# Performance work log

Hardware: AMD Instinct MI355X
Metric: run time of the kernel (lower is better)

## Reference

```python
import jax, jax.numpy as jnp
import numpy as np

HEAD_SIZE = 64
N_EMBD = 128
B, T = 16, 2048


def setup_inputs() -> dict:
    key = jax.random.key(0)
    ks = jax.random.split(key, 7)
    s = 1.0 / np.sqrt(N_EMBD)
    return {
        "x": jax.random.normal(ks[0], (B, T, N_EMBD), dtype=jnp.float32),
        "Wk": jax.random.normal(ks[1], (N_EMBD, HEAD_SIZE), dtype=jnp.float32) * s,
        "bk": jax.random.normal(ks[2], (HEAD_SIZE,), dtype=jnp.float32) * s,
        "Wq": jax.random.normal(ks[3], (N_EMBD, HEAD_SIZE), dtype=jnp.float32) * s,
        "bq": jax.random.normal(ks[4], (HEAD_SIZE,), dtype=jnp.float32) * s,
        "Wv": jax.random.normal(ks[5], (N_EMBD, HEAD_SIZE), dtype=jnp.float32) * s,
        "bv": jax.random.normal(ks[6], (HEAD_SIZE,), dtype=jnp.float32) * s,
    }


def reference(x, Wk, bk, Wq, bq, Wv, bv):
    # x: [B, T, C]; single-head causal attention (dropout in eval mode = identity)
    Tdim = x.shape[1]
    k = x @ Wk + bk  # [B, T, H]
    q = x @ Wq + bq  # [B, T, H]
    v = x @ Wv + bv  # [B, T, H]
    scale = jnp.asarray(k.shape[-1], x.dtype) ** -0.5
    wei = jnp.einsum("bth,bsh->bts", q, k) * scale  # [B, T, T]
    causal = jnp.tril(jnp.ones((Tdim, Tdim), dtype=bool))
    wei = jnp.where(causal, wei, -jnp.inf)
    wei = jax.nn.softmax(wei, axis=-1)
    out = jnp.einsum("bts,bsh->bth", wei, v)  # [B, T, H]
    return out
```

## Files before the change

kernel.cpp:

```cpp
#include <hip/hip_runtime.h>
#include <hip/hip_bf16.h>
#include <math.h>

#define HS 64
#define NE 128
#define TSEQ 2048

typedef short s8v __attribute__((ext_vector_type(8)));
typedef float f4v __attribute__((ext_vector_type(4)));

__device__ __forceinline__ unsigned short f2bf(float f) {
    unsigned int u = __float_as_uint(f);
    u += 0x7FFFu + ((u >> 16) & 1u);
    return (unsigned short)(u >> 16);
}

__device__ __forceinline__ unsigned int pkbf(float a, float b) {
    union { __hip_bfloat162 h; unsigned int u; } cv;
    cv.h = __float22bfloat162_rn(make_float2(a, b));
    return cv.u;
}

__device__ __forceinline__ s8v mk_s8v(unsigned int a, unsigned int b,
                                      unsigned int c, unsigned int d) {
    union { unsigned int u[4]; s8v v; } cv;
    cv.u[0] = a; cv.u[1] = b; cv.u[2] = c; cv.u[3] = d;
    return cv.v;
}

__device__ __forceinline__ float fexp2(float x) {
    float r;
    asm("v_exp_f32 %0, %1" : "=v"(r) : "v"(x));
    return r;
}

__device__ __forceinline__ void glds16(const unsigned short* g, unsigned short* l) {
    __builtin_amdgcn_global_load_lds(
        (const __attribute__((address_space(1))) unsigned int*)g,
        (__attribute__((address_space(3))) unsigned int*)l,
        16, 0, 0);
}

__global__ __launch_bounds__(256) void wconv(
    const float* __restrict__ Wq, const float* __restrict__ Wk,
    const float* __restrict__ Wv, unsigned short* __restrict__ wt)
{
    const int g = blockIdx.x * 256 + threadIdx.x;
    const int lane = g & 63;
    const int mtks = g >> 6;
    const int mt = mtks >> 2;
    const int ks = mtks & 3;
    const int li = lane & 15;
    const int quad = lane >> 4;
    const int m = mt * 16 + li;
    const int mat = m >> 6;
    const int n = m & 63;
    const int k0 = ks * 32 + quad * 8;
    const float* W = (mat == 0) ? Wq : (mat == 1) ? Wk : Wv;
    const float s = (mat == 0) ? 0.18033688f : 1.0f;

    unsigned int u[4];
#pragma unroll
    for (int h = 0; h < 4; ++h)
        u[h] = pkbf(W[(k0 + 2 * h) * HS + n] * s, W[(k0 + 2 * h + 1) * HS + n] * s);
    *(s8v*)(wt + (size_t)g * 8) = mk_s8v(u[0], u[1], u[2], u[3]);
}

__global__ __launch_bounds__(64) void qkv(
    const float* __restrict__ x, const unsigned short* __restrict__ wt,
    const float* __restrict__ bq, const float* __restrict__ bk,
    const float* __restrict__ bv,
    unsigned short* __restrict__ qo, unsigned short* __restrict__ ko,
    unsigned short* __restrict__ vt)
{
    const int tid = threadIdx.x;
    const int quad = tid >> 4;
    const int li = tid & 15;
    const size_t t0 = (size_t)blockIdx.x * 16;
    const size_t t = t0 + li;

    s8v xb[4];
    const float* xr = x + t * NE + quad * 8;
#pragma unroll
    for (int ks = 0; ks < 4; ++ks) {
        float4 f0 = *(const float4*)(xr + ks * 32);
        float4 f1 = *(const float4*)(xr + ks * 32 + 4);
        xb[ks] = mk_s8v(pkbf(f0.x, f0.y), pkbf(f0.z, f0.w),
                        pkbf(f1.x, f1.y), pkbf(f1.z, f1.w));
    }

    f4v acc[12];
#pragma unroll
    for (int mt = 0; mt < 12; ++mt) acc[mt] = (f4v){0.f, 0.f, 0.f, 0.f};

#pragma unroll
    for (int mt = 0; mt < 12; ++mt) {
#pragma unroll
        for (int ks = 0; ks < 4; ++ks) {
            s8v af = *(const s8v*)(wt + ((mt * 4 + ks) << 9) + tid * 8);
            acc[mt] = __builtin_amdgcn_mfma_f32_16x16x32_bf16(af, xb[ks], acc[mt], 0, 0, 0);
        }
    }

    const int d0 = quad * 4;
    const float sq = 0.18033688f;

#pragma unroll
    for (int mt = 0; mt < 4; ++mt) {
        float4 bb = *(const float4*)(bq + mt * 16 + d0);
        *(ushort4*)(qo + t * HS + mt * 16 + d0) = (ushort4){
            f2bf(acc[mt][0] + bb.x * sq), f2bf(acc[mt][1] + bb.y * sq),
            f2bf(acc[mt][2] + bb.z * sq), f2bf(acc[mt][3] + bb.w * sq)};
    }
#pragma unroll
    for (int mt = 0; mt < 4; ++mt) {
        float4 bb = *(const float4*)(bk + mt * 16 + d0);
        *(ushort4*)(ko + t * HS + mt * 16 + d0) = (ushort4){
            f2bf(acc[mt + 4][0] + bb.x), f2bf(acc[mt + 4][1] + bb.y),
            f2bf(acc[mt + 4][2] + bb.z), f2bf(acc[mt + 4][3] + bb.w)};
    }
    const size_t bidx = t0 >> 11;
    const size_t trow = t & 2047;
#pragma unroll
    for (int mt = 0; mt < 4; ++mt) {
        float4 bb = *(const float4*)(bv + mt * 16 + d0);
#pragma unroll
        for (int r = 0; r < 4; ++r) {
            vt[(bidx * HS + mt * 16 + d0 + r) * TSEQ + trow] =
                f2bf(acc[mt + 8][r] + (&bb.x)[r]);
        }
    }
}

__global__ __launch_bounds__(256) void attn_main(
    const unsigned short* __restrict__ qb,
    const unsigned short* __restrict__ kb,
    const unsigned short* __restrict__ vtb,
    float* __restrict__ out, float* __restrict__ pbuf, float* __restrict__ lsbuf)
{
    __shared__ unsigned short Ks[2][64 * 64];
    __shared__ unsigned short Vs[2][64 * 64];
    __shared__ __align__(16) unsigned short Ps[4][1024];

    const int tid = threadIdx.x;
    const int w = tid >> 6;
    const int lane = tid & 63;
    const int quad = lane >> 4;
    const int li = lane & 15;

    const int id = blockIdx.x;
    const int b = id / 80;
    const int u = 79 - (id - b * 80);
    int qt, c, nc;
    if (u < 8)       { qt = u;                 c = 0;            nc = 1; }
    else if (u < 24) { qt = 8 + ((u - 8) >> 1);  c = (u - 8) & 1;  nc = 2; }
    else if (u < 48) { qt = 16 + (u - 24) / 3;   c = (u - 24) % 3; nc = 3; }
    else             { qt = 24 + ((u - 48) >> 2); c = (u - 48) & 3; nc = 4; }
    const int tb = c * 8;
    const int te_ = tb + 8;
    const int te = (te_ < qt + 1) ? te_ : (qt + 1);

    const size_t base = (size_t)b * TSEQ;
    const int t0 = qt << 6;
    const int qrow = t0 + w * 16 + li;

    const unsigned short* qrp = qb + (base + qrow) * HS + quad * 8;
    s8v qf0 = *(const s8v*)qrp;
    s8v qf1 = *(const s8v*)(qrp + 32);

    const int rA = w * 8 + (lane >> 3);
    const int csw = (lane & 7) ^ (rA & 7);
    const unsigned short* kgA = kb + (base + rA) * HS + csw * 8;
    const unsigned short* kgB = kgA + 32 * HS;
    const unsigned short* vgA = vtb + ((size_t)b * HS + rA) * TSEQ + csw * 8;
    const unsigned short* vgB = vgA + 32 * TSEQ;
    const int ldsA = w * 512 + lane * 8;
    const int ldsB = 2048 + w * 512 + lane * 8;

    glds16(kgA + (size_t)tb * 4096, &Ks[0][ldsA]);
    glds16(kgB + (size_t)tb * 4096, &Ks[0][ldsB]);
    glds16(vgA + (size_t)tb * 64,   &Vs[0][ldsA]);
    glds16(vgB + (size_t)tb * 64,   &Vs[0][ldsB]);

    f4v c_o[4];
#pragma unroll
    for (int f = 0; f < 4; ++f) c_o[f] = (f4v){0.f, 0.f, 0.f, 0.f};
    float lsum = 0.f;

    char* pbse = (char*)&Ps[w][0];
    const int swz0 = (quad ^ (li & 7)) * 8;
    const int swz1 = ((4 + quad) ^ (li & 7)) * 8;

    __syncthreads();

    for (int tl = tb; tl < te; ++tl) {
        const int bi = (tl - tb) & 1;
        if (tl + 1 < te) {
            const int nb = bi ^ 1;
            glds16(kgA + (size_t)(tl + 1) * 4096, &Ks[nb][ldsA]);
            glds16(kgB + (size_t)(tl + 1) * 4096, &Ks[nb][ldsB]);
            glds16(vgA + (size_t)(tl + 1) * 64,   &Vs[nb][ldsA]);
            glds16(vgB + (size_t)(tl + 1) * 64,   &Vs[nb][ldsB]);
        }
        const unsigned short* Kc = &Ks[bi][0];
        const unsigned short* Vc = &Vs[bi][0];
        const bool diag = (tl == qt);

        float pr[4][4];
        float rs = 0.f;
#pragma unroll
        for (int kt = 0; kt < 4; ++kt) {
            const unsigned short* krow = Kc + (kt * 16 + li) * 64;
            s8v k0 = *(const s8v*)(krow + swz0);
            s8v k1 = *(const s8v*)(krow + swz1);
            f4v cst = (f4v){0.f, 0.f, 0.f, 0.f};
            cst = __builtin_amdgcn_mfma_f32_16x16x32_bf16(k0, qf0, cst, 0, 0, 0);
            cst = __builtin_amdgcn_mfma_f32_16x16x32_bf16(k1, qf1, cst, 0, 0, 0);
            if (diag) {
                const int key0 = (tl << 6) + kt * 16 + quad * 4;
#pragma unroll
                for (int rr = 0; rr < 4; ++rr)
                    if (key0 + rr > qrow) cst[rr] = -INFINITY;
            }
#pragma unroll
            for (int rr = 0; rr < 4; ++rr) {
                pr[kt][rr] = fexp2(cst[rr]);
                rs += pr[kt][rr];
            }
        }
        lsum += rs;

#pragma unroll
        for (int kt = 0; kt < 4; ++kt) {
            *(uint2*)(pbse + (kt * 2 + (quad >> 1)) * 256 + li * 16 + (quad & 1) * 8) =
                make_uint2(pkbf(pr[kt][0], pr[kt][1]), pkbf(pr[kt][2], pr[kt][3]));
        }
        s8v pf0 = *(const s8v*)(pbse + lane * 16);
        s8v pf1 = *(const s8v*)(pbse + 1024 + lane * 16);

#pragma unroll
        for (int f = 0; f < 4; ++f) {
            const unsigned short* vrow = Vc + (f * 16 + li) * 64;
            s8v v0 = *(const s8v*)(vrow + swz0);
            s8v v1 = *(const s8v*)(vrow + swz1);
            c_o[f] = __builtin_amdgcn_mfma_f32_16x16x32_bf16(v0, pf0, c_o[f], 0, 0, 0);
            c_o[f] = __builtin_amdgcn_mfma_f32_16x16x32_bf16(v1, pf1, c_o[f], 0, 0, 0);
        }

        __syncthreads();
    }

    lsum += __shfl_xor(lsum, 16);
    lsum += __shfl_xor(lsum, 32);

    if (nc == 1) {
        const float inv = 1.0f / lsum;
        float* orow = out + (base + qrow) * HS + quad * 4;
#pragma unroll
        for (int f = 0; f < 4; ++f) {
            f4v res = c_o[f];
            res[0] *= inv; res[1] *= inv; res[2] *= inv; res[3] *= inv;
            *(f4v*)(orow + f * 16) = res;
        }
    } else {
        const int local = (qt < 16) ? (qt - 8) * 2 + c
                        : (qt < 24) ? 16 + (qt - 16) * 3 + c
                                    : 40 + (qt - 24) * 4 + c;
        const int pidx = b * 72 + local;
        float* pc = pbuf + (size_t)pidx * 4096 + (w * 16 + li) * 64;
#pragma unroll
        for (int f = 0; f < 4; ++f)
            *(f4v*)(pc + f * 16 + quad * 4) = c_o[f];
        if (quad == 0)
            lsbuf[(size_t)pidx * 64 + w * 16 + li] = lsum;
    }
}

__global__ __launch_bounds__(256) void attn_reduce(
    const float* __restrict__ pbuf, const float* __restrict__ lsbuf,
    float* __restrict__ out)
{
    const int g = blockIdx.x;
    const int b = g / 24;
    const int r = g - b * 24;
    int qt, lbase, nc;
    if (r < 8)       { qt = 8 + r;        lbase = 2 * r;            nc = 2; }
    else if (r < 16) { qt = 16 + (r - 8); lbase = 16 + 3 * (r - 8); nc = 3; }
    else             { qt = 24 + (r - 16); lbase = 40 + 4 * (r - 16); nc = 4; }
    const int pidx0 = b * 72 + lbase;

    const int tid = threadIdx.x;
    const int row = tid >> 2;
    const int seg = tid & 3;

    float4 acc[4];
#pragma unroll
    for (int j = 0; j < 4; ++j) acc[j] = make_float4(0.f, 0.f, 0.f, 0.f);
    float ls = 0.f;

    for (int cc = 0; cc < nc; ++cc) {
        const float* pc = pbuf + (size_t)(pidx0 + cc) * 4096 + row * 64 + seg * 16;
#pragma unroll
        for (int j = 0; j < 4; ++j) {
            float4 v = *(const float4*)(pc + j * 4);
            acc[j].x += v.x; acc[j].y += v.y; acc[j].z += v.z; acc[j].w += v.w;
        }
        ls += lsbuf[(size_t)(pidx0 + cc) * 64 + row];
    }
    const float inv = 1.0f / ls;
    float* orow = out + ((size_t)b * TSEQ + (qt << 6) + row) * HS + seg * 16;
#pragma unroll
    for (int j = 0; j < 4; ++j) {
        *(float4*)(orow + j * 4) = make_float4(acc[j].x * inv, acc[j].y * inv,
                                               acc[j].z * inv, acc[j].w * inv);
    }
}

extern "C" void kernel_launch(void* const* d_in, const int* in_sizes, int n_in,
                              void* d_out, int out_size, void* d_ws, size_t ws_size,
                              hipStream_t stream) {
    const float* x  = (const float*)d_in[0];
    const float* Wk = (const float*)d_in[1];
    const float* bk = (const float*)d_in[2];
    const float* Wq = (const float*)d_in[3];
    const float* bq = (const float*)d_in[4];
    const float* Wv = (const float*)d_in[5];
    const float* bv = (const float*)d_in[6];
    float* outp = (float*)d_out;

    const size_t elems = (size_t)16 * TSEQ * HS;
    unsigned short* qbuf = (unsigned short*)d_ws;
    unsigned short* kbuf = qbuf + elems;
    unsigned short* vbuf = kbuf + elems;
    unsigned short* wtb  = vbuf + elems;
    float* pbuf  = (float*)(wtb + 32768);
    float* lsbuf = pbuf + (size_t)1152 * 4096;

    wconv<<<12, 256, 0, stream>>>(Wq, Wk, Wv, wtb);
    qkv<<<2048, 64, 0, stream>>>(x, wtb, bq, bk, bv, qbuf, kbuf, vbuf);
    attn_main<<<1280, 256, 0, stream>>>(qbuf, kbuf, vbuf, outp, pbuf, lsbuf);
    attn_reduce<<<384, 256, 0, stream>>>(pbuf, lsbuf, outp);
}
```

Measured before the change: 117.3 us.

## Fuse split-KV reduction into attention kernel via last-block atomic counter

Removes the separate attn_reduce launch. Each split block writes its partials, fences, and atomically increments a per-query-tile counter, and the last-arriving block sums the partials and writes the output. The counters are zeroed in the wconv kernel. This saves a kernel launch and its tail, at the cost of an atomic, a fence, and a serial reduction done by the last block of each tile.

```diff
diff --git a/kernel.cpp b/kernel.cpp
--- a/kernel.cpp
+++ b/kernel.cpp
@@ -43,9 +43,11 @@
 
 __global__ __launch_bounds__(256) void wconv(
     const float* __restrict__ Wq, const float* __restrict__ Wk,
-    const float* __restrict__ Wv, unsigned short* __restrict__ wt)
+    const float* __restrict__ Wv, unsigned short* __restrict__ wt,
+    unsigned int* __restrict__ cnt)
 {
     const int g = blockIdx.x * 256 + threadIdx.x;
+    if (g < 384) cnt[g] = 0u;
     const int lane = g & 63;
     const int mtks = g >> 6;
     const int mt = mtks >> 2;
@@ -136,11 +138,13 @@
     const unsigned short* __restrict__ qb,
     const unsigned short* __restrict__ kb,
     const unsigned short* __restrict__ vtb,
-    float* __restrict__ out, float* __restrict__ pbuf, float* __restrict__ lsbuf)
+    float* __restrict__ out, float* __restrict__ pbuf, float* __restrict__ lsbuf,
+    unsigned int* __restrict__ cnt)
 {
     __shared__ unsigned short Ks[2][64 * 64];
     __shared__ unsigned short Vs[2][64 * 64];
     __shared__ __align__(16) unsigned short Ps[4][1024];
+    __shared__ int is_last;
 
     const int tid = threadIdx.x;
     const int w = tid >> 6;
@@ -262,57 +266,60 @@
             res[0] *= inv; res[1] *= inv; res[2] *= inv; res[3] *= inv;
             *(f4v*)(orow + f * 16) = res;
         }
-    } else {
-        const int local = (qt < 16) ? (qt - 8) * 2 + c
-                        : (qt < 24) ? 16 + (qt - 16) * 3 + c
-                                    : 40 + (qt - 24) * 4 + c;
-        const int pidx = b * 72 + local;
-        float* pc = pbuf + (size_t)pidx * 4096 + (w * 16 + li) * 64;
-#pragma unroll
-        for (int f = 0; f < 4; ++f)
-            *(f4v*)(pc + f * 16 + quad * 4) = c_o[f];
-        if (quad == 0)
-            lsbuf[(size_t)pidx * 64 + w * 16 + li] = lsum;
-    }
-}
-
-__global__ __launch_bounds__(256) void attn_reduce(
-    const float* __restrict__ pbuf, const float* __restrict__ lsbuf,
-    float* __restrict__ out)
-{
-    const int g = blockIdx.x;
-    const int b = g / 24;
-    const int r = g - b * 24;
-    int qt, lbase, nc;
-    if (r < 8)       { qt = 8 + r;        lbase = 2 * r;            nc = 2; }
-    else if (r < 16) { qt = 16 + (r - 8); lbase = 16 + 3 * (r - 8); nc = 3; }
-    else             { qt = 24 + (r - 16); lbase = 40 + 4 * (r - 16); nc = 4; }
+        return;
+    }
+
+    const int local = (qt < 16) ? (qt - 8) * 2 + c
+                    : (qt < 24) ? 16 + (qt - 16) * 3 + c
+                                : 40 + (qt - 24) * 4 + c;
+    const int pidx = b * 72 + local;
+    float* pc = pbuf + (size_t)pidx * 4096 + (w * 16 + li) * 64;
+#pragma unroll
+    for (int f = 0; f < 4; ++f)
+        *(f4v*)(pc + f * 16 + quad * 4) = c_o[f];
+    if (quad == 0)
+        lsbuf[(size_t)pidx * 64 + w * 16 + li] = lsum;
+
+    __threadfence();
+    __syncthreads();
+    const int ridx = (qt < 16) ? (qt - 8)
+                   : (qt < 24) ? 8 + (qt - 16)
+                               : 16 + (qt - 24);
+    if (tid == 0) {
+        unsigned int old = atomicAdd(&cnt[b * 24 + ridx], 1u);
+        is_last = (old == (unsigned int)(nc - 1)) ? 1 : 0;
+    }
+    __syncthreads();
+    if (!is_last) return;
+
+    __threadfence();
+    const int lbase = (qt < 16) ? 2 * (qt - 8)
+                    : (qt < 24) ? 16 + 3 * (qt - 16)
+                                : 40 + 4 * (qt - 24);
     const int pidx0 = b * 72 + lbase;
-
-    const int tid = threadIdx.x;
     const int row = tid >> 2;
     const int seg = tid & 3;
 
-    float4 acc[4];
-#pragma unroll
-    for (int j = 0; j < 4; ++j) acc[j] = make_float4(0.f, 0.f, 0.f, 0.f);
+    float4 racc[4];
+#pragma unroll
+    for (int j = 0; j < 4; ++j) racc[j] = make_float4(0.f, 0.f, 0.f, 0.f);
     float ls = 0.f;
 
     for (int cc = 0; cc < nc; ++cc) {
-        const float* pc = pbuf + (size_t)(pidx0 + cc) * 4096 + row * 64 + seg * 16;
+        const float* ps = pbuf + (size_t)(pidx0 + cc) * 4096 + row * 64 + seg * 16;
 #pragma unroll
         for (int j = 0; j < 4; ++j) {
-            float4 v = *(const float4*)(pc + j * 4);
-            acc[j].x += v.x; acc[j].y += v.y; acc[j].z += v.z; acc[j].w += v.w;
+            float4 v = *(const float4*)(ps + j * 4);
+            racc[j].x += v.x; racc[j].y += v.y; racc[j].z += v.z; racc[j].w += v.w;
         }
         ls += lsbuf[(size_t)(pidx0 + cc) * 64 + row];
     }
     const float inv = 1.0f / ls;
-    float* orow = out + ((size_t)b * TSEQ + (qt << 6) + row) * HS + seg * 16;
+    float* orow = out + (base + t0 + row) * HS + seg * 16;
 #pragma unroll
     for (int j = 0; j < 4; ++j) {
-        *(float4*)(orow + j * 4) = make_float4(acc[j].x * inv, acc[j].y * inv,
-                                               acc[j].z * inv, acc[j].w * inv);
+        *(float4*)(orow + j * 4) = make_float4(racc[j].x * inv, racc[j].y * inv,
+                                               racc[j].z * inv, racc[j].w * inv);
     }
 }
 
@@ -335,9 +342,9 @@
     unsigned short* wtb  = vbuf + elems;
     float* pbuf  = (float*)(wtb + 32768);
     float* lsbuf = pbuf + (size_t)1152 * 4096;
-
-    wconv<<<12, 256, 0, stream>>>(Wq, Wk, Wv, wtb);
+    unsigned int* cntb = (unsigned int*)(lsbuf + (size_t)1152 * 64);
+
+    wconv<<<12, 256, 0, stream>>>(Wq, Wk, Wv, wtb, cntb);
     qkv<<<2048, 64, 0, stream>>>(x, wtb, bq, bk, bv, qbuf, kbuf, vbuf);
-    attn_main<<<1280, 256, 0, stream>>>(qbuf, kbuf, vbuf, outp, pbuf, lsbuf);
-    attn_reduce<<<384, 256, 0, stream>>>(pbuf, lsbuf, outp);
-}
+    attn_main<<<1280, 256, 0, stream>>>(qbuf, kbuf, vbuf, outp, pbuf, lsbuf, cntb);
+}
```

After: 347.4 us. +196.1%, slower.
